# Optimization experiments

Measured on AMD Instinct MI355X. Metric: run time of the kernel, lower is better.

The kernel has to match this reference:

```python
import jax, jax.numpy as jnp
import numpy as np

jax.config.update("jax_enable_x64", True)  # original casts to double for covpool/SVD

BN_EPS = 1e-5


def setup_inputs() -> dict:
    key = jax.random.key(0)
    k1, k2 = jax.random.split(key)
    x = jax.random.normal(k1, (64, 2048, 14, 14), dtype=jnp.float32)
    conv_w = jax.random.normal(k2, (256, 2048), dtype=jnp.float32) * 0.02  # 1x1 conv kernel
    bn_gamma = jnp.ones((256,), dtype=jnp.float32)
    bn_beta = jnp.zeros((256,), dtype=jnp.float32)
    return {"x": x, "conv_w": conv_w, "bn_gamma": bn_gamma, "bn_beta": bn_beta}


def reference(x, conv_w, bn_gamma, bn_beta):
    # --- dimension reduction block: 1x1 conv (no bias) + BN (train mode) + ReLU ---
    y = jnp.einsum('oc,bchw->bohw', conv_w, x)  # [B,256,14,14]
    mean = y.mean(axis=(0, 2, 3), keepdims=True)
    var = y.var(axis=(0, 2, 3), keepdims=True)
    y = (y - mean) * jax.lax.rsqrt(var + BN_EPS)
    y = y * bn_gamma[None, :, None, None] + bn_beta[None, :, None, None]
    y = jnp.maximum(y, 0.0)

    # --- Covpool: x @ (I/M - 11^T/M^2) @ x^T, in float64 as original ---
    B, d, h, w = y.shape
    M = h * w
    z = y.reshape(B, d, M).astype(jnp.float64)
    zc = z - z.mean(axis=2, keepdims=True)          # centering == multiplying by I_hat
    cov = jnp.einsum('bim,bjm->bij', zc, zc) / M    # [B,d,d], symmetric PSD

    # --- Eigen decomposition (SVD of symmetric PSD == eigh), clamp tiny eigvals ---
    s, V = jnp.linalg.eigh(cov)                     # s: [B,d], V: [B,d,d]
    eps = jnp.finfo(jnp.float64).eps
    s = jnp.maximum(s, eps)

    # --- Power: matrix square root Q = V sqrt(S) V^T ---
    Q = jnp.einsum('bij,bj,bkj->bik', V, jnp.sqrt(s), V)  # [B,d,d]

    # --- upper-triangular (incl. diag) vectorization, row-major like torch triu ---
    iu = jnp.triu_indices(d)
    q_triv = Q[:, iu[0], iu[1]]                     # [B, d*(d+1)/2]
    return q_triv.astype(jnp.float32)
```

## Files before the change

### kernel.cpp

```cpp
#include <hip/hip_runtime.h>
#include <hip/hip_bf16.h>

static constexpr int B   = 64;
static constexpr int CIN = 2048;
static constexpr int O   = 256;
static constexpr int HW  = 196;
static constexpr int D   = 256;
static constexpr int TRI = 32896;
static constexpr int NQ_COUPLED = 5;
static constexpr int NTILE = 10;
static constexpr size_t NELEM = (size_t)B * D * D;
static constexpr size_t YN    = (size_t)B * O * HW;

typedef unsigned short u16;
typedef unsigned short u16x8 __attribute__((ext_vector_type(8)));
typedef __bf16         bf16x8 __attribute__((ext_vector_type(8)));
typedef float          f32x4 __attribute__((ext_vector_type(4)));

__constant__ int c_TI[NTILE] = {0,0,0,0,1,1,1,2,2,3};
__constant__ int c_TJ[NTILE] = {0,1,2,3,1,2,3,2,3,3};

static __device__ __forceinline__ u16 f2bf(float x) {
    unsigned int u = __float_as_uint(x);
    u += 0x7FFFu + ((u >> 16) & 1u);
    return (u16)(u >> 16);
}
static __device__ __forceinline__ float bf2f(u16 h) {
    return __uint_as_float(((unsigned int)h) << 16);
}
static __device__ __forceinline__ f32x4 mm_bf16(u16x8 a, u16x8 b, f32x4 c) {
    return __builtin_amdgcn_mfma_f32_16x16x32_bf16(
        __builtin_bit_cast(bf16x8, a), __builtin_bit_cast(bf16x8, b), c, 0, 0, 0);
}

__global__ __launch_bounds__(256) void k_wsplit(const float* __restrict__ W,
                                                u16* __restrict__ Wh,
                                                u16* __restrict__ Wl) {
    const size_t i = (size_t)blockIdx.x * 256 + threadIdx.x;
    const float v = W[i];
    const u16 h = f2bf(v);
    Wh[i] = h;
    Wl[i] = f2bf(v - bf2f(h));
}

__global__ __launch_bounds__(256) void k_conv(const float* __restrict__ x,
                                              const u16* __restrict__ Wh,
                                              const u16* __restrict__ Wl,
                                              float* __restrict__ psum) {
    const int l   = blockIdx.x;
    const int xcd = l & 7, idx = l >> 3;
    const int p   = xcd + 8 * (idx >> 2);
    const int ot  = idx & 3;
    const int ct  = p >> 2, ks = p & 3;
    const int o0  = ot * 64;
    const int cbase = ks * 512;
    float* yp = psum + (size_t)ks * YN;

    const int tid = threadIdx.x;

    __shared__ u16 sWh[64][40], sWl[64][40];
    __shared__ u16 sXh[64][40], sXl[64][40];
    __shared__ int s_coff[64];
    __shared__ int s_yoff[64];

    if (tid < 64) {
        const int g = ct * 64 + tid;
        const int b = g / 196;
        const int m = g - b * 196;
        s_coff[tid] = b * (CIN * HW) + m;
        s_yoff[tid] = b * (O * HW) + m;
    }
    __syncthreads();

    const int rW  = tid >> 2, kqW = (tid & 3) << 3;
    const int cX  = tid & 63, kqX = (tid >> 6) << 3;
    const int cofX = s_coff[cX];

    const int lane = tid & 63, w = tid >> 6;
    const int wr = w >> 1, wc = w & 1;
    const int lr = lane & 15, lg = lane >> 4;

    const f32x4 z4 = {0.f, 0.f, 0.f, 0.f};
    f32x4 acc00 = z4, acc01 = z4, acc10 = z4, acc11 = z4;

    for (int kb = 0; kb < 512; kb += 32) {
        {
            const size_t g = (size_t)(o0 + rW) * CIN + cbase + kb + kqW;
            *(u16x8*)&sWh[rW][kqW] = *(const u16x8*)&Wh[g];
            *(u16x8*)&sWl[rW][kqW] = *(const u16x8*)&Wl[g];
        }
        {
            u16x8 vh, vl;
            #pragma unroll
            for (int i = 0; i < 8; ++i) {
                const float v = x[(size_t)(cbase + kb + kqX + i) * HW + cofX];
                const u16 h = f2bf(v);
                vh[i] = h;
                vl[i] = f2bf(v - bf2f(h));
            }
            *(u16x8*)&sXh[cX][kqX] = vh;
            *(u16x8*)&sXl[cX][kqX] = vl;
        }
        __syncthreads();

        const int ra = wr * 32 + lr, rb = wc * 32 + lr;
        const int ko = lg << 3;
        const u16x8 a0h = *(const u16x8*)&sWh[ra][ko];
        const u16x8 a0l = *(const u16x8*)&sWl[ra][ko];
        const u16x8 a1h = *(const u16x8*)&sWh[ra + 16][ko];
        const u16x8 a1l = *(const u16x8*)&sWl[ra + 16][ko];
        const u16x8 b0h = *(const u16x8*)&sXh[rb][ko];
        const u16x8 b0l = *(const u16x8*)&sXl[rb][ko];
        const u16x8 b1h = *(const u16x8*)&sXh[rb + 16][ko];
        const u16x8 b1l = *(const u16x8*)&sXl[rb + 16][ko];

        acc00 = mm_bf16(a0h, b0h, acc00);
        acc00 = mm_bf16(a0h, b0l, acc00);
        acc00 = mm_bf16(a0l, b0h, acc00);
        acc01 = mm_bf16(a0h, b1h, acc01);
        acc01 = mm_bf16(a0h, b1l, acc01);
        acc01 = mm_bf16(a0l, b1h, acc01);
        acc10 = mm_bf16(a1h, b0h, acc10);
        acc10 = mm_bf16(a1h, b0l, acc10);
        acc10 = mm_bf16(a1l, b0h, acc10);
        acc11 = mm_bf16(a1h, b1h, acc11);
        acc11 = mm_bf16(a1h, b1l, acc11);
        acc11 = mm_bf16(a1l, b1h, acc11);
        __syncthreads();
    }

    auto epi = [&](const f32x4& a, int fi, int fj) {
        const int orow0 = o0 + wr * 32 + fi * 16 + (lg << 2);
        const int col   = wc * 32 + fj * 16 + lr;
        const int yo = s_yoff[col];
        #pragma unroll
        for (int r = 0; r < 4; ++r)
            yp[(size_t)(orow0 + r) * HW + yo] = a[r];
    };
    epi(acc00, 0, 0); epi(acc01, 0, 1); epi(acc10, 1, 0); epi(acc11, 1, 1);
}

__global__ __launch_bounds__(256) void k_redy(const float* __restrict__ ps,
                                              float* __restrict__ y) {
    const size_t i = ((size_t)blockIdx.x * 256 + threadIdx.x) * 4;
    if (i >= YN) return;
    float4 a = *(const float4*)&ps[i];
    const float4 b = *(const float4*)&ps[YN + i];
    const float4 c = *(const float4*)&ps[2 * YN + i];
    const float4 d = *(const float4*)&ps[3 * YN + i];
    a.x += b.x + c.x + d.x; a.y += b.y + c.y + d.y;
    a.z += b.z + c.z + d.z; a.w += b.w + c.w + d.w;
    *(float4*)&y[i] = a;
}

__global__ __launch_bounds__(256) void k_bnstats(const float* __restrict__ y,
                                                 const float* __restrict__ gamma,
                                                 const float* __restrict__ beta,
                                                 float* __restrict__ scl,
                                                 float* __restrict__ shf) {
    const int o = blockIdx.x;
    const int tid = threadIdx.x;
    float s = 0.f, s2 = 0.f;
    if (tid < HW) {
        for (int b = 0; b < B; ++b) {
            const float v = y[((size_t)b * O + o) * HW + tid];
            s += v; s2 += v * v;
        }
    }
    #pragma unroll
    for (int msk = 32; msk; msk >>= 1) {
        s  += __shfl_xor(s,  msk);
        s2 += __shfl_xor(s2, msk);
    }
    __shared__ float rs[4], rs2[4];
    if ((tid & 63) == 0) { rs[tid >> 6] = s; rs2[tid >> 6] = s2; }
    __syncthreads();
    if (tid == 0) {
        const float N = (float)(B * HW);
        const float ts  = rs[0] + rs[1] + rs[2] + rs[3];
        const float ts2 = rs2[0] + rs2[1] + rs2[2] + rs2[3];
        const float mean = ts / N;
        const float var  = ts2 / N - mean * mean;
        const float sc = gamma[o] * rsqrtf(var + 1e-5f);
        scl[o] = sc;
        shf[o] = beta[o] - mean * sc;
    }
}

__global__ __launch_bounds__(64) void k_center(float* __restrict__ z,
                                               const float* __restrict__ scl,
                                               const float* __restrict__ shf) {
    const int row = blockIdx.x;
    const int o = row & 255;
    const int lane = threadIdx.x;
    const float sc = scl[o], sh = shf[o];
    float* zr = &z[(size_t)row * HW];
    float vals[4];
    float s = 0.f;
    #pragma unroll
    for (int q = 0; q < 4; ++q) {
        const int m = q * 64 + lane;
        float v = 0.f;
        if (m < HW) v = fmaxf(fmaf(zr[m], sc, sh), 0.f);
        vals[q] = v; s += v;
    }
    #pragma unroll
    for (int msk = 32; msk; msk >>= 1) s += __shfl_xor(s, msk);
    const float mean = s / (float)HW;
    #pragma unroll
    for (int q = 0; q < 4; ++q) {
        const int m = q * 64 + lane;
        if (m < HW) zr[m] = vals[q] - mean;
    }
}

__global__ __launch_bounds__(256) void k_cov(const float* __restrict__ z,
                                             double* __restrict__ cov) {
    const int b = blockIdx.y;
    const int jt = blockIdx.x & 3, it = blockIdx.x >> 2;
    const int i0 = it * 64, j0 = jt * 64;
    const int tid = threadIdx.x;
    const int tn = tid & 15, tmq = tid >> 4;

    __shared__ float sA[28][68], sB[28][68];
    double acc[4][4] = {};
    const float* zb = &z[(size_t)b * D * HW];

    for (int k0 = 0; k0 < HW; k0 += 28) {
        #pragma unroll
        for (int q = 0; q < 7; ++q) {
            const int idx = tid + q * 256;
            const int r = idx / 28, kk = idx % 28;
            sA[kk][r] = zb[(size_t)(i0 + r) * HW + k0 + kk];
            sB[kk][r] = zb[(size_t)(j0 + r) * HW + k0 + kk];
        }
        __syncthreads();
        #pragma unroll
        for (int kk = 0; kk < 28; ++kk) {
            const float4 av = *reinterpret_cast<const float4*>(&sA[kk][tmq << 2]);
            const float4 bv = *reinterpret_cast<const float4*>(&sB[kk][tn << 2]);
            const double aa[4] = {av.x, av.y, av.z, av.w};
            const double bb[4] = {bv.x, bv.y, bv.z, bv.w};
            #pragma unroll
            for (int i = 0; i < 4; ++i)
                #pragma unroll
                for (int j = 0; j < 4; ++j)
                    acc[i][j] = fma(aa[i], bb[j], acc[i][j]);
        }
        __syncthreads();
    }
    const double inv = 1.0 / (double)HW;
    #pragma unroll
    for (int i = 0; i < 4; ++i)
        #pragma unroll
        for (int j = 0; j < 4; ++j)
            cov[(size_t)b * D * D + (size_t)(i0 + (tmq << 2) + i) * D
                + j0 + (tn << 2) + j] = acc[i][j] * inv;
}

__global__ __launch_bounds__(256) void k_lmax(const double* __restrict__ cov,
                                              double* __restrict__ cn) {
    const int b = blockIdx.x;
    const int tid = threadIdx.x;
    const double* A = &cov[(size_t)b * D * D];
    __shared__ double v[256];
    __shared__ double red[4];
    v[tid] = 1.0;
    __syncthreads();
    double lam = 1.0;
    for (int it = 0; it < 6; ++it) {
        const double* row = &A[(size_t)tid * D];
        double u0 = 0.0, u1 = 0.0;
        #pragma unroll 16
        for (int k = 0; k < D; k += 2) {
            const double2 rv = *(const double2*)&row[k];
            u0 = fma(rv.x, v[k], u0);
            u1 = fma(rv.y, v[k + 1], u1);
        }
        const double u = u0 + u1;
        double s = u * u;
        #pragma unroll
        for (int msk = 32; msk; msk >>= 1) s += __shfl_xor(s, msk);
        if ((tid & 63) == 0) red[tid >> 6] = s;
        __syncthreads();
        const double nrm = sqrt(red[0] + red[1] + red[2] + red[3]) + 1e-300;
        lam = nrm;
        __syncthreads();
        v[tid] = u / nrm;
        __syncthreads();
    }
    if (tid == 0) cn[b] = (lam > 1e-30) ? 1.25 * lam : 1.0;
}

__global__ __launch_bounds__(256) void k_init(const double* __restrict__ cov,
                                              const double* __restrict__ cn,
                                              u16* __restrict__ Yh,
                                              u16* __restrict__ Yl) {
    const size_t e = (size_t)blockIdx.x * 256 + threadIdx.x;
    const int b = (int)(e >> 16);
    const int ij = (int)(e & 65535);
    const int i = ij >> 8, j = ij & 255;
    const double diag = (i == j) ? 1e-7 : 0.0;
    const float f = (float)(cov[e] / cn[b] + diag);
    const u16 h = f2bf(f);
    Yh[e] = h;
    Yl[e] = f2bf(f - bf2f(h));
}

template <int MODE, int FUSED>
__global__ __launch_bounds__(256) void k_mgemm(
        const u16* __restrict__ A0h, const u16* __restrict__ A0l,
        const u16* __restrict__ B0h, const u16* __restrict__ B0l,
        u16* __restrict__ C0h, u16* __restrict__ C0l,
        const u16* __restrict__ A1h, const u16* __restrict__ A1l,
        const u16* __restrict__ B1h, const u16* __restrict__ B1l,
        u16* __restrict__ C1h, u16* __restrict__ C1l,
        const double* __restrict__ cn, float* __restrict__ outp) {
    const int orig = blockIdx.x;
    const int xcd  = orig & 7;
    const int s    = orig >> 3;
    int batch, tile, opz;
    if (FUSED) {
        const int bl  = s / 20;
        const int rem = s - bl * 20;
        opz  = rem >= 10;
        tile = rem - opz * 10;
        batch = xcd * 8 + bl;
    } else {
        opz = 0;
        batch = xcd * 8 + s / 10;
        tile = s - (s / 10) * 10;
    }

    const u16 *Ah, *Al, *Bh, *Bl;
    u16 *Ch, *Cl;
    if (opz == 0) { Ah = A0h; Al = A0l; Bh = B0h; Bl = B0l; Ch = C0h; Cl = C0l; }
    else          { Ah = A1h; Al = A1l; Bh = B1h; Bl = B1l; Ch = C1h; Cl = C1l; }

    const int it = c_TI[tile], jt = c_TJ[tile];
    const int i0 = it * 64, j0 = jt * 64;
    const size_t boff = (size_t)batch * 65536;
    Ah += boff; Al += boff; Bh += boff; Bl += boff; Ch += boff; Cl += boff;

    const int tid = threadIdx.x;
    __shared__ u16 sA[2][2][64][40];
    __shared__ u16 sB[2][2][64][40];

    const int rW = tid >> 2, kq = (tid & 3) << 3;
    const u16* gAh = Ah + (size_t)(i0 + rW) * 256 + kq;
    const u16* gAl = Al + (size_t)(i0 + rW) * 256 + kq;
    const u16* gBh = Bh + (size_t)(j0 + rW) * 256 + kq;
    const u16* gBl = Bl + (size_t)(j0 + rW) * 256 + kq;

    const int lane = tid & 63, w = tid >> 6;
    const int wr = w >> 1, wc = w & 1;
    const int lr = lane & 15, lg = lane >> 4, ko = lg << 3;
    const int ra = wr * 32 + lr, rb = wc * 32 + lr;

    const f32x4 z4 = {0.f, 0.f, 0.f, 0.f};
    f32x4 acc00 = z4, acc01 = z4, acc10 = z4, acc11 = z4;

    *(u16x8*)&sA[0][0][rW][kq] = *(const u16x8*)&gAh[0];
    *(u16x8*)&sA[0][1][rW][kq] = *(const u16x8*)&gAl[0];
    *(u16x8*)&sB[0][0][rW][kq] = *(const u16x8*)&gBh[0];
    *(u16x8*)&sB[0][1][rW][kq] = *(const u16x8*)&gBl[0];
    __syncthreads();

    int cur = 0;
    #pragma unroll
    for (int st = 0; st < 8; ++st) {
        u16x8 nAh, nAl, nBh, nBl;
        if (st < 7) {
            const int k1 = (st + 1) << 5;
            nAh = *(const u16x8*)&gAh[k1];
            nAl = *(const u16x8*)&gAl[k1];
            nBh = *(const u16x8*)&gBh[k1];
            nBl = *(const u16x8*)&gBl[k1];
        }
        const u16x8 a0h = *(const u16x8*)&sA[cur][0][ra][ko];
        const u16x8 a0l = *(const u16x8*)&sA[cur][1][ra][ko];
        const u16x8 a1h = *(const u16x8*)&sA[cur][0][ra + 16][ko];
        const u16x8 a1l = *(const u16x8*)&sA[cur][1][ra + 16][ko];
        const u16x8 b0h = *(const u16x8*)&sB[cur][0][rb][ko];
        const u16x8 b0l = *(const u16x8*)&sB[cur][1][rb][ko];
        const u16x8 b1h = *(const u16x8*)&sB[cur][0][rb + 16][ko];
        const u16x8 b1l = *(const u16x8*)&sB[cur][1][rb + 16][ko];

        acc00 = mm_bf16(a0h, b0h, acc00);
        acc00 = mm_bf16(a0h, b0l, acc00);
        acc00 = mm_bf16(a0l, b0h, acc00);
        acc01 = mm_bf16(a0h, b1h, acc01);
        acc01 = mm_bf16(a0h, b1l, acc01);
        acc01 = mm_bf16(a0l, b1h, acc01);
        acc10 = mm_bf16(a1h, b0h, acc10);
        acc10 = mm_bf16(a1h, b0l, acc10);
        acc10 = mm_bf16(a1l, b0h, acc10);
        acc11 = mm_bf16(a1h, b1h, acc11);
        acc11 = mm_bf16(a1h, b1l, acc11);
        acc11 = mm_bf16(a1l, b1h, acc11);

        if (st < 7) {
            *(u16x8*)&sA[cur ^ 1][0][rW][kq] = nAh;
            *(u16x8*)&sA[cur ^ 1][1][rW][kq] = nAl;
            *(u16x8*)&sB[cur ^ 1][0][rW][kq] = nBh;
            *(u16x8*)&sB[cur ^ 1][1][rW][kq] = nBl;
        }
        __syncthreads();
        cur ^= 1;
    }

    const f32x4 accs[2][2] = {{acc00, acc01}, {acc10, acc11}};
    const int orow = wr * 32 + (lg << 2);
    const int ocol = wc * 32 + lr;

    if (MODE == 3) {
        const double sc = sqrt(cn[batch]);
        #pragma unroll
        for (int fi = 0; fi < 2; ++fi)
            #pragma unroll
            for (int r = 0; r < 4; ++r) {
                const int gi = i0 + orow + fi * 16 + r;
                const size_t rowoff = (size_t)gi * D - ((size_t)gi * (gi - 1)) / 2;
                #pragma unroll
                for (int fj = 0; fj < 2; ++fj) {
                    const int gj = j0 + ocol + fj * 16;
                    if (gj >= gi)
                        outp[(size_t)batch * TRI + rowoff + (gj - gi)] =
                            (float)(sc * (double)accs[fi][fj][r]);
                }
            }
        return;
    }

    u16 hv[2][4][2], lv[2][4][2];
    #pragma unroll
    for (int fi = 0; fi < 2; ++fi)
        #pragma unroll
        for (int r = 0; r < 4; ++r) {
            const int li = orow + fi * 16 + r;
            const int gi = i0 + li;
            #pragma unroll
            for (int fj = 0; fj < 2; ++fj) {
                const int gj = j0 + ocol + fj * 16;
                float v = accs[fi][fj][r];
                if (MODE == 1) {
                    const size_t xo = (size_t)gi * 256 + gj;
                    const float xv = bf2f(Ah[xo]) + bf2f(Al[xo]);
                    v = (((gi == gj) ? 15.0f : 0.0f) - 10.0f * xv + 3.0f * v) * 0.125f;
                }
                const u16 h = f2bf(v);
                const u16 l = f2bf(v - bf2f(h));
                const size_t co = (size_t)gi * 256 + gj;
                Ch[co] = h;
                Cl[co] = l;
                hv[fi][r][fj] = h;
                lv[fi][r][fj] = l;
            }
        }

    if (it != jt) {
        u16 (*tH)[72] = reinterpret_cast<u16(*)[72]>(&sA[0][0][0][0]);
        u16 (*tL)[72] = reinterpret_cast<u16(*)[72]>(&sB[0][0][0][0]);
        #pragma unroll
        for (int fi = 0; fi < 2; ++fi)
            #pragma unroll
            for (int r = 0; r < 4; ++r) {
                const int li = orow + fi * 16 + r;
                #pragma unroll
                for (int fj = 0; fj < 2; ++fj) {
                    const int lj = ocol + fj * 16;
                    tH[lj][li] = hv[fi][r][fj];
                    tL[lj][li] = lv[fi][r][fj];
                }
            }
        __syncthreads();
        const int r2 = tid >> 2, c2 = (tid & 3) << 4;
        const size_t mo = (size_t)(j0 + r2) * 256 + i0 + c2;
        *(u16x8*)&Ch[mo]     = *(const u16x8*)&tH[r2][c2];
        *(u16x8*)&Ch[mo + 8] = *(const u16x8*)&tH[r2][c2 + 8];
        *(u16x8*)&Cl[mo]     = *(const u16x8*)&tL[r2][c2];
        *(u16x8*)&Cl[mo + 8] = *(const u16x8*)&tL[r2][c2 + 8];
    }
}

extern "C" void kernel_launch(void* const* d_in, const int* in_sizes, int n_in,
                              void* d_out, int out_size, void* d_ws, size_t ws_size,
                              hipStream_t stream) {
    const float* x     = (const float*)d_in[0];
    const float* W     = (const float*)d_in[1];
    const float* gamma = (const float*)d_in[2];
    const float* beta  = (const float*)d_in[3];
    float* out = (float*)d_out;

    char* ws = (char*)d_ws;
    size_t off = 0;
    auto alloc = [&](size_t bytes) -> void* {
        void* p = ws + off;
        off += (bytes + 255) & ~(size_t)255;
        return p;
    };
    float*  y    = (float*)alloc(YN * sizeof(float));
    double* cov  = (double*)alloc(NELEM * sizeof(double));
    float*  scl  = (float*)alloc(O * sizeof(float));
    float*  shf  = (float*)alloc(O * sizeof(float));
    double* cn   = (double*)alloc(B * sizeof(double));
    u16*    Wh   = (u16*)alloc((size_t)O * CIN * sizeof(u16));
    u16*    Wl   = (u16*)alloc((size_t)O * CIN * sizeof(u16));
    u16* pl = (u16*)alloc(12 * NELEM * sizeof(u16));
    if (off > ws_size) return;
    u16 *YAh = pl,             *YAl = pl + NELEM;
    u16 *YBh = pl + 2 * NELEM, *YBl = pl + 3 * NELEM;
    u16 *MAh = pl + 4 * NELEM, *MAl = pl + 5 * NELEM;
    u16 *MBh = pl + 6 * NELEM, *MBl = pl + 7 * NELEM;
    u16 *Rh  = pl + 8 * NELEM, *Rl  = pl + 9 * NELEM;
    u16 *Uh  = pl + 10 * NELEM,*Ul  = pl + 11 * NELEM;
    float* psum = (float*)pl;

    k_wsplit <<<(O * CIN) / 256, 256, 0, stream>>>(W, Wh, Wl);
    k_conv   <<<3136, 256, 0, stream>>>(x, Wh, Wl, psum);
    k_redy   <<<3136, 256, 0, stream>>>(psum, y);
    k_bnstats<<<O, 256, 0, stream>>>(y, gamma, beta, scl, shf);
    k_center <<<B * O, 64, 0, stream>>>(y, scl, shf);
    k_cov    <<<dim3(16, B), 256, 0, stream>>>(y, cov);
    k_lmax   <<<B, 256, 0, stream>>>(cov, cn);
    k_init   <<<B * 256, 256, 0, stream>>>(cov, cn, YAh, YAl);

    k_mgemm<1, 0><<<640, 256, 0, stream>>>(YAh, YAl, YAh, YAl, Rh, Rl,
                                           YAh, YAl, YAh, YAl, Rh, Rl, cn, out);
    k_mgemm<2, 0><<<640, 256, 0, stream>>>(YAh, YAl, Rh, Rl, YBh, YBl,
                                           YAh, YAl, Rh, Rl, YBh, YBl, cn, out);
    k_mgemm<2, 0><<<640, 256, 0, stream>>>(Rh, Rl, YBh, YBl, MBh, MBl,
                                           Rh, Rl, YBh, YBl, MBh, MBl, cn, out);

    u16 *Ych = YBh, *Ycl = YBl, *Yah = YAh, *Yal = YAl;
    u16 *Mch = MBh, *Mcl = MBl, *Mah = MAh, *Mal = MAl;
    for (int itq = 0; itq < NQ_COUPLED; ++itq) {
        k_mgemm<1, 0><<<640, 256, 0, stream>>>(Mch, Mcl, Mch, Mcl, Rh, Rl,
                                               Mch, Mcl, Mch, Mcl, Rh, Rl, cn, out);
        k_mgemm<2, 1><<<1280, 256, 0, stream>>>(Ych, Ycl, Rh, Rl, Yah, Yal,
                                                Mch, Mcl, Rh, Rl, Uh, Ul, cn, out);
        k_mgemm<2, 0><<<640, 256, 0, stream>>>(Rh, Rl, Uh, Ul, Mah, Mal,
                                               Rh, Rl, Uh, Ul, Mah, Mal, cn, out);
        u16* t;
        t = Ych; Ych = Yah; Yah = t;  t = Ycl; Ycl = Yal; Yal = t;
        t = Mch; Mch = Mah; Mah = t;  t = Mcl; Mcl = Mal; Mal = t;
    }
    k_mgemm<1, 0><<<640, 256, 0, stream>>>(Mch, Mcl, Mch, Mcl, Rh, Rl,
                                           Mch, Mcl, Mch, Mcl, Rh, Rl, cn, out);
    k_mgemm<3, 0><<<640, 256, 0, stream>>>(Ych, Ycl, Rh, Rl, Uh, Ul,
                                           Ych, Ycl, Rh, Rl, Uh, Ul, cn, out);
}
```

Baseline: 552.4 us.

## Enlarge conv and Newton-Schulz GEMM tiles to 128x128 with 64-wide K stages

Both the 1x1-conv GEMM and the batched Newton-Schulz GEMMs move from 64x64 tiles with K=32 to 128x128 tiles with K=64 stages, giving each wave a 4x4 grid of MFMA fragments. The mgemm kernel no longer exploits symmetry: it drops the 10 upper-triangle tiles plus transposed mirror stores and computes all four 128x128 quadrants directly. Grid sizes shrink accordingly, and the conv kernel gets a register-prefetch pipeline. The goal is more reuse of each shared-memory fragment and fewer blocks. In exchange the kernels need more registers and much larger LDS tiles, which may limit occupancy, and the GEMMs do more MFMA work now that symmetry is no longer used.

```diff
diff --git a/kernel.cpp b/kernel.cpp
--- a/kernel.cpp
+++ b/kernel.cpp
@@ -8,17 +8,14 @@
 static constexpr int D   = 256;
 static constexpr int TRI = 32896;
 static constexpr int NQ_COUPLED = 5;
-static constexpr int NTILE = 10;
 static constexpr size_t NELEM = (size_t)B * D * D;
 static constexpr size_t YN    = (size_t)B * O * HW;
 
 typedef unsigned short u16;
+typedef unsigned short u16x4 __attribute__((ext_vector_type(4)));
 typedef unsigned short u16x8 __attribute__((ext_vector_type(8)));
 typedef __bf16         bf16x8 __attribute__((ext_vector_type(8)));
 typedef float          f32x4 __attribute__((ext_vector_type(4)));
-
-__constant__ int c_TI[NTILE] = {0,0,0,0,1,1,1,2,2,3};
-__constant__ int c_TJ[NTILE] = {0,1,2,3,1,2,3,2,3,3};
 
 static __device__ __forceinline__ u16 f2bf(float x) {
     unsigned int u = __float_as_uint(x);
@@ -43,101 +40,131 @@
     Wl[i] = f2bf(v - bf2f(h));
 }
 
-__global__ __launch_bounds__(256) void k_conv(const float* __restrict__ x,
-                                              const u16* __restrict__ Wh,
-                                              const u16* __restrict__ Wl,
-                                              float* __restrict__ psum) {
+__global__ __launch_bounds__(256, 2) void k_conv(const float* __restrict__ x,
+                                                 const u16* __restrict__ Wh,
+                                                 const u16* __restrict__ Wl,
+                                                 float* __restrict__ psum) {
     const int l   = blockIdx.x;
-    const int xcd = l & 7, idx = l >> 3;
-    const int p   = xcd + 8 * (idx >> 2);
-    const int ot  = idx & 3;
-    const int ct  = p >> 2, ks = p & 3;
-    const int o0  = ot * 64;
+    const int xcd = l & 7, u = l >> 3;
+    const int q   = xcd * 98 + u;
+    const int ks  = q & 3;
+    const int t2  = q >> 2;
+    const int ot  = t2 & 1, gt = t2 >> 1;
+    const int o0  = ot * 128;
     const int cbase = ks * 512;
     float* yp = psum + (size_t)ks * YN;
 
     const int tid = threadIdx.x;
 
-    __shared__ u16 sWh[64][40], sWl[64][40];
-    __shared__ u16 sXh[64][40], sXl[64][40];
-    __shared__ int s_coff[64];
-    __shared__ int s_yoff[64];
-
-    if (tid < 64) {
-        const int g = ct * 64 + tid;
-        const int b = g / 196;
-        const int m = g - b * 196;
-        s_coff[tid] = b * (CIN * HW) + m;
-        s_yoff[tid] = b * (O * HW) + m;
-    }
-    __syncthreads();
-
-    const int rW  = tid >> 2, kqW = (tid & 3) << 3;
-    const int cX  = tid & 63, kqX = (tid >> 6) << 3;
-    const int cofX = s_coff[cX];
+    __shared__ u16 sW[2][128][72], sX[2][128][72];
+
+    const int colX  = tid & 127;
+    const int chalf = (tid >> 7) * 32;
+    const int gX = gt * 128 + colX;
+    const int bX = gX / 196;
+    const int mX = gX - bX * 196;
+    const size_t xbase = (size_t)bX * (CIN * HW) + mX;
+
+    const int rW = tid >> 1, kh = (tid & 1) * 32;
+    const u16* gWh = Wh + (size_t)(o0 + rW) * CIN + cbase + kh;
+    const u16* gWl = Wl + (size_t)(o0 + rW) * CIN + cbase + kh;
 
     const int lane = tid & 63, w = tid >> 6;
     const int wr = w >> 1, wc = w & 1;
-    const int lr = lane & 15, lg = lane >> 4;
-
-    const f32x4 z4 = {0.f, 0.f, 0.f, 0.f};
-    f32x4 acc00 = z4, acc01 = z4, acc10 = z4, acc11 = z4;
-
-    for (int kb = 0; kb < 512; kb += 32) {
-        {
-            const size_t g = (size_t)(o0 + rW) * CIN + cbase + kb + kqW;
-            *(u16x8*)&sWh[rW][kqW] = *(const u16x8*)&Wh[g];
-            *(u16x8*)&sWl[rW][kqW] = *(const u16x8*)&Wl[g];
-        }
-        {
-            u16x8 vh, vl;
-            #pragma unroll
-            for (int i = 0; i < 8; ++i) {
-                const float v = x[(size_t)(cbase + kb + kqX + i) * HW + cofX];
+    const int lr = lane & 15, lg = lane >> 4, ko = lg << 3;
+
+    f32x4 acc[4][4] = {};
+
+    u16x8 pWh[4], pWl[4];
+    float pX[32];
+    u16x4 cXh[8], cXl[8];
+
+    auto loadW = [&](int kb) {
+        #pragma unroll
+        for (int qq = 0; qq < 4; ++qq) {
+            pWh[qq] = *(const u16x8*)&gWh[kb + qq * 8];
+            pWl[qq] = *(const u16x8*)&gWl[kb + qq * 8];
+        }
+    };
+    auto loadX = [&](int kb) {
+        #pragma unroll
+        for (int i = 0; i < 32; ++i)
+            pX[i] = x[xbase + (size_t)(cbase + kb + chalf + i) * HW];
+    };
+    auto convX = [&]() {
+        #pragma unroll
+        for (int i = 0; i < 32; i += 4) {
+            u16x4 vh, vl;
+            #pragma unroll
+            for (int j = 0; j < 4; ++j) {
+                const float v = pX[i + j];
                 const u16 h = f2bf(v);
-                vh[i] = h;
-                vl[i] = f2bf(v - bf2f(h));
+                vh[j] = h;
+                vl[j] = f2bf(v - bf2f(h));
             }
-            *(u16x8*)&sXh[cX][kqX] = vh;
-            *(u16x8*)&sXl[cX][kqX] = vl;
-        }
-        __syncthreads();
-
-        const int ra = wr * 32 + lr, rb = wc * 32 + lr;
-        const int ko = lg << 3;
-        const u16x8 a0h = *(const u16x8*)&sWh[ra][ko];
-        const u16x8 a0l = *(const u16x8*)&sWl[ra][ko];
-        const u16x8 a1h = *(const u16x8*)&sWh[ra + 16][ko];
-        const u16x8 a1l = *(const u16x8*)&sWl[ra + 16][ko];
-        const u16x8 b0h = *(const u16x8*)&sXh[rb][ko];
-        const u16x8 b0l = *(const u16x8*)&sXl[rb][ko];
-        const u16x8 b1h = *(const u16x8*)&sXh[rb + 16][ko];
-        const u16x8 b1l = *(const u16x8*)&sXl[rb + 16][ko];
-
-        acc00 = mm_bf16(a0h, b0h, acc00);
-        acc00 = mm_bf16(a0h, b0l, acc00);
-        acc00 = mm_bf16(a0l, b0h, acc00);
-        acc01 = mm_bf16(a0h, b1h, acc01);
-        acc01 = mm_bf16(a0h, b1l, acc01);
-        acc01 = mm_bf16(a0l, b1h, acc01);
-        acc10 = mm_bf16(a1h, b0h, acc10);
-        acc10 = mm_bf16(a1h, b0l, acc10);
-        acc10 = mm_bf16(a1l, b0h, acc10);
-        acc11 = mm_bf16(a1h, b1h, acc11);
-        acc11 = mm_bf16(a1h, b1l, acc11);
-        acc11 = mm_bf16(a1l, b1h, acc11);
-        __syncthreads();
-    }
-
-    auto epi = [&](const f32x4& a, int fi, int fj) {
-        const int orow0 = o0 + wr * 32 + fi * 16 + (lg << 2);
-        const int col   = wc * 32 + fj * 16 + lr;
-        const int yo = s_yoff[col];
-        #pragma unroll
-        for (int r = 0; r < 4; ++r)
-            yp[(size_t)(orow0 + r) * HW + yo] = a[r];
-    };
-    epi(acc00, 0, 0); epi(acc01, 0, 1); epi(acc10, 1, 0); epi(acc11, 1, 1);
+            cXh[i >> 2] = vh;
+            cXl[i >> 2] = vl;
+        }
+    };
+    auto storeWX = [&]() {
+        #pragma unroll
+        for (int qq = 0; qq < 4; ++qq) {
+            *(u16x8*)&sW[0][rW][kh + qq * 8] = pWh[qq];
+            *(u16x8*)&sW[1][rW][kh + qq * 8] = pWl[qq];
+        }
+        #pragma unroll
+        for (int qq = 0; qq < 8; ++qq) {
+            *(u16x4*)&sX[0][colX][chalf + qq * 4] = cXh[qq];
+            *(u16x4*)&sX[1][colX][chalf + qq * 4] = cXl[qq];
+        }
+    };
+    auto compute = [&]() {
+        #pragma unroll
+        for (int kr = 0; kr < 2; ++kr) {
+            const int kk = kr * 32 + ko;
+            u16x8 fah[4], fal[4], fbh[4], fbl[4];
+            #pragma unroll
+            for (int f = 0; f < 4; ++f) {
+                fah[f] = *(const u16x8*)&sW[0][wr * 64 + f * 16 + lr][kk];
+                fal[f] = *(const u16x8*)&sW[1][wr * 64 + f * 16 + lr][kk];
+                fbh[f] = *(const u16x8*)&sX[0][wc * 64 + f * 16 + lr][kk];
+                fbl[f] = *(const u16x8*)&sX[1][wc * 64 + f * 16 + lr][kk];
+            }
+            #pragma unroll
+            for (int fi = 0; fi < 4; ++fi)
+                #pragma unroll
+                for (int fj = 0; fj < 4; ++fj) {
+                    acc[fi][fj] = mm_bf16(fah[fi], fbh[fj], acc[fi][fj]);
+                    acc[fi][fj] = mm_bf16(fah[fi], fbl[fj], acc[fi][fj]);
+                    acc[fi][fj] = mm_bf16(fal[fi], fbh[fj], acc[fi][fj]);
+                }
+        }
+    };
+
+    loadW(0); loadX(0); convX();
+    for (int st = 0; st < 8; ++st) {
+        __syncthreads();
+        storeWX();
+        __syncthreads();
+        if (st < 7) { loadW((st + 1) * 64); loadX((st + 1) * 64); }
+        compute();
+        if (st < 7) convX();
+    }
+
+    #pragma unroll
+    for (int fj = 0; fj < 4; ++fj) {
+        const int gcol = gt * 128 + wc * 64 + fj * 16 + lr;
+        const int bb = gcol / 196;
+        const int mm = gcol - bb * 196;
+        const size_t ybase = (size_t)bb * (O * HW) + mm;
+        #pragma unroll
+        for (int fi = 0; fi < 4; ++fi)
+            #pragma unroll
+            for (int r = 0; r < 4; ++r) {
+                const int orow = o0 + wr * 64 + fi * 16 + (lg << 2) + r;
+                yp[ybase + (size_t)orow * HW] = acc[fi][fj][r];
+            }
+    }
 }
 
 __global__ __launch_bounds__(256) void k_redy(const float* __restrict__ ps,
@@ -308,7 +335,7 @@
 }
 
 template <int MODE, int FUSED>
-__global__ __launch_bounds__(256) void k_mgemm(
+__global__ __launch_bounds__(256, 2) void k_mgemm(
         const u16* __restrict__ A0h, const u16* __restrict__ A0l,
         const u16* __restrict__ B0h, const u16* __restrict__ B0l,
         u16* __restrict__ C0h, u16* __restrict__ C0l,
@@ -319,17 +346,17 @@
     const int orig = blockIdx.x;
     const int xcd  = orig & 7;
     const int s    = orig >> 3;
-    int batch, tile, opz;
+    int batch, quad, opz;
     if (FUSED) {
-        const int bl  = s / 20;
-        const int rem = s - bl * 20;
-        opz  = rem >= 10;
-        tile = rem - opz * 10;
+        const int bl  = s >> 3;
+        const int opq = s & 7;
+        opz  = opq >> 2;
+        quad = opq & 3;
         batch = xcd * 8 + bl;
     } else {
         opz = 0;
-        batch = xcd * 8 + s / 10;
-        tile = s - (s / 10) * 10;
+        batch = xcd * 8 + (s >> 2);
+        quad = s & 3;
     }
 
     const u16 *Ah, *Al, *Bh, *Bl;
@@ -337,150 +364,119 @@
     if (opz == 0) { Ah = A0h; Al = A0l; Bh = B0h; Bl = B0l; Ch = C0h; Cl = C0l; }
     else          { Ah = A1h; Al = A1l; Bh = B1h; Bl = B1l; Ch = C1h; Cl = C1l; }
 
-    const int it = c_TI[tile], jt = c_TJ[tile];
-    const int i0 = it * 64, j0 = jt * 64;
+    const int i0 = (quad >> 1) * 128, j0 = (quad & 1) * 128;
     const size_t boff = (size_t)batch * 65536;
     Ah += boff; Al += boff; Bh += boff; Bl += boff; Ch += boff; Cl += boff;
 
     const int tid = threadIdx.x;
-    __shared__ u16 sA[2][2][64][40];
-    __shared__ u16 sB[2][2][64][40];
-
-    const int rW = tid >> 2, kq = (tid & 3) << 3;
-    const u16* gAh = Ah + (size_t)(i0 + rW) * 256 + kq;
-    const u16* gAl = Al + (size_t)(i0 + rW) * 256 + kq;
-    const u16* gBh = Bh + (size_t)(j0 + rW) * 256 + kq;
-    const u16* gBl = Bl + (size_t)(j0 + rW) * 256 + kq;
+    __shared__ u16 sA[2][128][72], sB[2][128][72];
+
+    const int rW = tid >> 1, kh = (tid & 1) * 32;
+    const u16* gAh = Ah + (size_t)(i0 + rW) * 256 + kh;
+    const u16* gAl = Al + (size_t)(i0 + rW) * 256 + kh;
+    const u16* gBh = Bh + (size_t)(j0 + rW) * 256 + kh;
+    const u16* gBl = Bl + (size_t)(j0 + rW) * 256 + kh;
 
     const int lane = tid & 63, w = tid >> 6;
     const int wr = w >> 1, wc = w & 1;
     const int lr = lane & 15, lg = lane >> 4, ko = lg << 3;
-    const int ra = wr * 32 + lr, rb = wc * 32 + lr;
-
-    const f32x4 z4 = {0.f, 0.f, 0.f, 0.f};
-    f32x4 acc00 = z4, acc01 = z4, acc10 = z4, acc11 = z4;
-
-    *(u16x8*)&sA[0][0][rW][kq] = *(const u16x8*)&gAh[0];
-    *(u16x8*)&sA[0][1][rW][kq] = *(const u16x8*)&gAl[0];
-    *(u16x8*)&sB[0][0][rW][kq] = *(const u16x8*)&gBh[0];
-    *(u16x8*)&sB[0][1][rW][kq] = *(const u16x8*)&gBl[0];
-    __syncthreads();
-
-    int cur = 0;
-    #pragma unroll
-    for (int st = 0; st < 8; ++st) {
-        u16x8 nAh, nAl, nBh, nBl;
-        if (st < 7) {
-            const int k1 = (st + 1) << 5;
-            nAh = *(const u16x8*)&gAh[k1];
-            nAl = *(const u16x8*)&gAl[k1];
-            nBh = *(const u16x8*)&gBh[k1];
-            nBl = *(const u16x8*)&gBl[k1];
-        }
-        const u16x8 a0h = *(const u16x8*)&sA[cur][0][ra][ko];
-        const u16x8 a0l = *(const u16x8*)&sA[cur][1][ra][ko];
-        const u16x8 a1h = *(const u16x8*)&sA[cur][0][ra + 16][ko];
-        const u16x8 a1l = *(const u16x8*)&sA[cur][1][ra + 16][ko];
-        const u16x8 b0h = *(const u16x8*)&sB[cur][0][rb][ko];
-        const u16x8 b0l = *(const u16x8*)&sB[cur][1][rb][ko];
-        const u16x8 b1h = *(const u16x8*)&sB[cur][0][rb + 16][ko];
-        const u16x8 b1l = *(const u16x8*)&sB[cur][1][rb + 16][ko];
-
-        acc00 = mm_bf16(a0h, b0h, acc00);
-        acc00 = mm_bf16(a0h, b0l, acc00);
-        acc00 = mm_bf16(a0l, b0h, acc00);
-        acc01 = mm_bf16(a0h, b1h, acc01);
-        acc01 = mm_bf16(a0h, b1l, acc01);
-        acc01 = mm_bf16(a0l, b1h, acc01);
-        acc10 = mm_bf16(a1h, b0h, acc10);
-        acc10 = mm_bf16(a1h, b0l, acc10);
-        acc10 = mm_bf16(a1l, b0h, acc10);
-        acc11 = mm_bf16(a1h, b1h, acc11);
-        acc11 = mm_bf16(a1h, b1l, acc11);
-        acc11 = mm_bf16(a1l, b1h, acc11);
-
-        if (st < 7) {
-            *(u16x8*)&sA[cur ^ 1][0][rW][kq] = nAh;
-            *(u16x8*)&sA[cur ^ 1][1][rW][kq] = nAl;
-            *(u16x8*)&sB[cur ^ 1][0][rW][kq] = nBh;
-            *(u16x8*)&sB[cur ^ 1][1][rW][kq] = nBl;
-        }
-        __syncthreads();
-        cur ^= 1;
-    }
-
-    const f32x4 accs[2][2] = {{acc00, acc01}, {acc10, acc11}};
-    const int orow = wr * 32 + (lg << 2);
-    const int ocol = wc * 32 + lr;
+
+    f32x4 acc[4][4] = {};
+
+    u16x8 pAh[4], pAl[4], pBh[4], pBl[4];
+    auto g_load = [&](int kb) {
+        #pragma unroll
+        for (int qq = 0; qq < 4; ++qq) {
+            pAh[qq] = *(const u16x8*)&gAh[kb + qq * 8];
+            pAl[qq] = *(const u16x8*)&gAl[kb + qq * 8];
+            pBh[qq] = *(const u16x8*)&gBh[kb + qq * 8];
+            pBl[qq] = *(const u16x8*)&gBl[kb + qq * 8];
+        }
+    };
+    auto s_store = [&]() {
+        #pragma unroll
+        for (int qq = 0; qq < 4; ++qq) {
+            *(u16x8*)&sA[0][rW][kh + qq * 8] = pAh[qq];
+            *(u16x8*)&sA[1][rW][kh + qq * 8] = pAl[qq];
+            *(u16x8*)&sB[0][rW][kh + qq * 8] = pBh[qq];
+            *(u16x8*)&sB[1][rW][kh + qq * 8] = pBl[qq];
+        }
+    };
+    auto compute = [&]() {
+        #pragma unroll
+        for (int kr = 0; kr < 2; ++kr) {
+            const int kk = kr * 32 + ko;
+            u16x8 fah[4], fal[4], fbh[4], fbl[4];
+            #pragma unroll
+            for (int f = 0; f < 4; ++f) {
+                fah[f] = *(const u16x8*)&sA[0][wr * 64 + f * 16 + lr][kk];
+                fal[f] = *(const u16x8*)&sA[1][wr * 64 + f * 16 + lr][kk];
+                fbh[f] = *(const u16x8*)&sB[0][wc * 64 + f * 16 + lr][kk];
+                fbl[f] = *(const u16x8*)&sB[1][wc * 64 + f * 16 + lr][kk];
+            }
+            #pragma unroll
+            for (int fi = 0; fi < 4; ++fi)
+                #pragma unroll
+                for (int fj = 0; fj < 4; ++fj) {
+                    acc[fi][fj] = mm_bf16(fah[fi], fbh[fj], acc[fi][fj]);
+                    acc[fi][fj] = mm_bf16(fah[fi], fbl[fj], acc[fi][fj]);
+                    acc[fi][fj] = mm_bf16(fal[fi], fbh[fj], acc[fi][fj]);
+                }
+        }
+    };
+
+    g_load(0);
+    for (int st = 0; st < 4; ++st) {
+        __syncthreads();
+        s_store();
+        __syncthreads();
+        if (st < 3) g_load((st + 1) * 64);
+        compute();
+    }
+
+    const int orow = wr * 64 + (lg << 2);
+    const int ocol = wc * 64 + lr;
 
     if (MODE == 3) {
         const double sc = sqrt(cn[batch]);
         #pragma unroll
-        for (int fi = 0; fi < 2; ++fi)
+        for (int fi = 0; fi < 4; ++fi)
             #pragma unroll
             for (int r = 0; r < 4; ++r) {
                 const int gi = i0 + orow + fi * 16 + r;
                 const size_t rowoff = (size_t)gi * D - ((size_t)gi * (gi - 1)) / 2;
                 #pragma unroll
-                for (int fj = 0; fj < 2; ++fj) {
+                for (int fj = 0; fj < 4; ++fj) {
                     const int gj = j0 + ocol + fj * 16;
                     if (gj >= gi)
                         outp[(size_t)batch * TRI + rowoff + (gj - gi)] =
-                            (float)(sc * (double)accs[fi][fj][r]);
+                            (float)(sc * (double)acc[fi][fj][r]);
                 }
             }
         return;
     }
 
-    u16 hv[2][4][2], lv[2][4][2];
-    #pragma unroll
-    for (int fi = 0; fi < 2; ++fi)
+    #pragma unroll
+    for (int fi = 0; fi < 4; ++fi)
         #pragma unroll
         for (int r = 0; r < 4; ++r) {
-            const int li = orow + fi * 16 + r;
-            const int gi = i0 + li;
-            #pragma unroll
-            for (int fj = 0; fj < 2; ++fj) {
+            const int gi = i0 + orow + fi * 16 + r;
+            #pragma unroll
+            for (int fj = 0; fj < 4; ++fj) {
                 const int gj = j0 + ocol + fj * 16;
-                float v = accs[fi][fj][r];
+                float v = acc[fi][fj][r];
                 if (MODE == 1) {
                     const size_t xo = (size_t)gi * 256 + gj;
                     const float xv = bf2f(Ah[xo]) + bf2f(Al[xo]);
                     v = (((gi == gj) ? 15.0f : 0.0f) - 10.0f * xv + 3.0f * v) * 0.125f;
                 }
                 const u16 h = f2bf(v);
-                const u16 l = f2bf(v - bf2f(h));
+                const u16 lo = f2bf(v - bf2f(h));
                 const size_t co = (size_t)gi * 256 + gj;
                 Ch[co] = h;
-                Cl[co] = l;
-                hv[fi][r][fj] = h;
-                lv[fi][r][fj] = l;
+                Cl[co] = lo;
             }
         }
-
-    if (it != jt) {
-        u16 (*tH)[72] = reinterpret_cast<u16(*)[72]>(&sA[0][0][0][0]);
-        u16 (*tL)[72] = reinterpret_cast<u16(*)[72]>(&sB[0][0][0][0]);
-        #pragma unroll
-        for (int fi = 0; fi < 2; ++fi)
-            #pragma unroll
-            for (int r = 0; r < 4; ++r) {
-                const int li = orow + fi * 16 + r;
-                #pragma unroll
-                for (int fj = 0; fj < 2; ++fj) {
-                    const int lj = ocol + fj * 16;
-                    tH[lj][li] = hv[fi][r][fj];
-                    tL[lj][li] = lv[fi][r][fj];
-                }
-            }
-        __syncthreads();
-        const int r2 = tid >> 2, c2 = (tid & 3) << 4;
-        const size_t mo = (size_t)(j0 + r2) * 256 + i0 + c2;
-        *(u16x8*)&Ch[mo]     = *(const u16x8*)&tH[r2][c2];
-        *(u16x8*)&Ch[mo + 8] = *(const u16x8*)&tH[r2][c2 + 8];
-        *(u16x8*)&Cl[mo]     = *(const u16x8*)&tL[r2][c2];
-        *(u16x8*)&Cl[mo + 8] = *(const u16x8*)&tL[r2][c2 + 8];
-    }
 }
 
 extern "C" void kernel_launch(void* const* d_in, const int* in_sizes, int n_in,
@@ -517,7 +513,7 @@
     float* psum = (float*)pl;
 
     k_wsplit <<<(O * CIN) / 256, 256, 0, stream>>>(W, Wh, Wl);
-    k_conv   <<<3136, 256, 0, stream>>>(x, Wh, Wl, psum);
+    k_conv   <<<784, 256, 0, stream>>>(x, Wh, Wl, psum);
     k_redy   <<<3136, 256, 0, stream>>>(psum, y);
     k_bnstats<<<O, 256, 0, stream>>>(y, gamma, beta, scl, shf);
     k_center <<<B * O, 64, 0, stream>>>(y, scl, shf);
@@ -525,28 +521,28 @@
     k_lmax   <<<B, 256, 0, stream>>>(cov, cn);
     k_init   <<<B * 256, 256, 0, stream>>>(cov, cn, YAh, YAl);
 
-    k_mgemm<1, 0><<<640, 256, 0, stream>>>(YAh, YAl, YAh, YAl, Rh, Rl,
+    k_mgemm<1, 0><<<256, 256, 0, stream>>>(YAh, YAl, YAh, YAl, Rh, Rl,
                                            YAh, YAl, YAh, YAl, Rh, Rl, cn, out);
-    k_mgemm<2, 0><<<640, 256, 0, stream>>>(YAh, YAl, Rh, Rl, YBh, YBl,
+    k_mgemm<2, 0><<<256, 256, 0, stream>>>(YAh, YAl, Rh, Rl, YBh, YBl,
                                            YAh, YAl, Rh, Rl, YBh, YBl, cn, out);
-    k_mgemm<2, 0><<<640, 256, 0, stream>>>(Rh, Rl, YBh, YBl, MBh, MBl,
+    k_mgemm<2, 0><<<256, 256, 0, stream>>>(Rh, Rl, YBh, YBl, MBh, MBl,
                                            Rh, Rl, YBh, YBl, MBh, MBl, cn, out);
 
     u16 *Ych = YBh, *Ycl = YBl, *Yah = YAh, *Yal = YAl;
     u16 *Mch = MBh, *Mcl = MBl, *Mah = MAh, *Mal = MAl;
     for (int itq = 0; itq < NQ_COUPLED; ++itq) {
-        k_mgemm<1, 0><<<640, 256, 0, stream>>>(Mch, Mcl, Mch, Mcl, Rh, Rl,
+        k_mgemm<1, 0><<<256, 256, 0, stream>>>(Mch, Mcl, Mch, Mcl, Rh, Rl,
                                                Mch, Mcl, Mch, Mcl, Rh, Rl, cn, out);
-        k_mgemm<2, 1><<<1280, 256, 0, stream>>>(Ych, Ycl, Rh, Rl, Yah, Yal,
-                                                Mch, Mcl, Rh, Rl, Uh, Ul, cn, out);
-        k_mgemm<2, 0><<<640, 256, 0, stream>>>(Rh, Rl, Uh, Ul, Mah, Mal,
+        k_mgemm<2, 1><<<512, 256, 0, stream>>>(Ych, Ycl, Rh, Rl, Yah, Yal,
+                                               Mch, Mcl, Rh, Rl, Uh, Ul, cn, out);
+        k_mgemm<2, 0><<<256, 256, 0, stream>>>(Rh, Rl, Uh, Ul, Mah, Mal,
                                                Rh, Rl, Uh, Ul, Mah, Mal, cn, out);
         u16* t;
         t = Ych; Ych = Yah; Yah = t;  t = Ycl; Ycl = Yal; Yal = t;
         t = Mch; Mch = Mah; Mah = t;  t = Mcl; Mcl = Mal; Mal = t;
     }
-    k_mgemm<1, 0><<<640, 256, 0, stream>>>(Mch, Mcl, Mch, Mcl, Rh, Rl,
+    k_mgemm<1, 0><<<256, 256, 0, stream>>>(Mch, Mcl, Mch, Mcl, Rh, Rl,
                                            Mch, Mcl, Mch, Mcl, Rh, Rl, cn, out);
-    k_mgemm<3, 0><<<640, 256, 0, stream>>>(Ych, Ycl, Rh, Rl, Uh, Ul,
+    k_mgemm<3, 0><<<256, 256, 0, stream>>>(Ych, Ycl, Rh, Rl, Uh, Ul,
                                            Ych, Ycl, Rh, Rl, Uh, Ul, cn, out);
 }
```

Result: slower. 588.7 us (+6.6%).
